# Kernel optimization log

Hardware: AMD Instinct MI355X
Metric: run time of the kernel (lower is better)

The kernel has to match this reference:

```python
import jax, jax.numpy as jnp
import numpy as np

# Module config
SIZE = (2, 2)
B, H, W, C = 16, 64, 64, 256


def setup_inputs() -> dict:
    key = jax.random.key(0)
    updates = jax.random.normal(key, (B, H, W, C), dtype=jnp.float32)
    OH, OW = H * SIZE[0], W * SIZE[1]
    # argmax-style mask: flat index into [OH, OW, C] (per-batch), pointing at the
    # top-left element of each pooling window (structure of max_pool_with_argmax)
    h = jnp.arange(H, dtype=jnp.int64)[:, None, None] * SIZE[0]   # [H,1,1]
    w = jnp.arange(W, dtype=jnp.int64)[None, :, None] * SIZE[1]   # [1,W,1]
    c = jnp.arange(C, dtype=jnp.int64)[None, None, :]             # [1,1,C]
    mask = (h * OW + w) * C + c                                   # [H,W,C]
    mask = jnp.broadcast_to(mask, (B, H, W, C))
    return {"updates": updates, "mask": mask}


def reference(updates, mask):
    # Faithful MaxUnpooling2D: scatter pooled values into upsampled output at
    # the positions given by the (per-batch flat) argmax mask; rest are zeros.
    Bv, Hv, Wv, Cv = updates.shape
    OH, OW = Hv * SIZE[0], Wv * SIZE[1]
    flat = OH * OW * Cv
    out = jnp.zeros((Bv, flat), dtype=updates.dtype)
    # tf.scatter_nd sums duplicates into a zero tensor; indices here are unique
    out = out.at[jnp.arange(Bv)[:, None], mask.reshape(Bv, -1)].add(
        updates.reshape(Bv, -1)
    )
    return out.reshape(Bv, OH, OW, Cv)
```

## Files before the change

kernel.cpp:

```cpp
#include <hip/hip_runtime.h>


constexpr int B = 16;
constexpr int H = 64, W = 64, C = 256;
constexpr int OH = 2 * H, OW = 2 * W;
constexpr long long OUT_PER_BATCH = (long long)OH * OW * C;
constexpr int N_THREADS = B * H * W * (C / 4);

typedef float f32x4 __attribute__((ext_vector_type(4)));
typedef int   i32x4 __attribute__((ext_vector_type(4)));

__global__ __launch_bounds__(256) void unpool_gather_kernel(
    const f32x4* __restrict__ upd4,
    const i32x4* __restrict__ mask4,
    float* __restrict__ out) {
    int i = blockIdx.x * blockDim.x + threadIdx.x;
    if (i >= N_THREADS) return;

    int c0 = (i & 63) << 2;
    int w  = (i >> 6) & 63;
    int h  = (i >> 12) & 63;
    int b  = i >> 18;

    i32x4 m = mask4[i];
    f32x4 u = upd4[i];

    float* obase = out + (long long)b * OUT_PER_BATCH;
    int oh = h << 1, ow = w << 1;

#pragma unroll
    for (int dy = 0; dy < 2; ++dy) {
#pragma unroll
        for (int dx = 0; dx < 2; ++dx) {
            int flat = ((oh + dy) * OW + (ow + dx)) * C + c0;
            f32x4 r;
            r.x = (m.x == flat)     ? u.x : 0.0f;
            r.y = (m.y == flat + 1) ? u.y : 0.0f;
            r.z = (m.z == flat + 2) ? u.z : 0.0f;
            r.w = (m.w == flat + 3) ? u.w : 0.0f;
            *(f32x4*)(obase + flat) = r;
        }
    }
}

extern "C" void kernel_launch(void* const* d_in, const int* in_sizes, int n_in,
                              void* d_out, int out_size, void* d_ws, size_t ws_size,
                              hipStream_t stream) {
    const f32x4* upd4  = (const f32x4*)d_in[0];
    const i32x4* mask4 = (const i32x4*)d_in[1];
    float*       out   = (float*)d_out;

    const int block = 256;
    const int grid  = N_THREADS / block;
    unpool_gather_kernel<<<grid, block, 0, stream>>>(upd4, mask4, out);
}
```

Baseline: 358.0 us.

## Switch to output-major grid-stride unpooling with contiguous vector stores

Each thread now owns one output quad and walks the output in a grid-stride loop over a fixed 2048-block grid, gathering the matching update and mask quad. Before, each thread read one input quad and wrote four scattered output quads. Now every store is perfectly contiguous across a wavefront, at the cost of reading each input quad four times (mostly from cache). The fixed grid also reduces block launch overhead.

Measured after the change: 371.2 us. 3.7% more time.

```diff
diff --git a/kernel.cpp b/kernel.cpp
--- a/kernel.cpp
+++ b/kernel.cpp
@@ -4,42 +4,38 @@
 constexpr int B = 16;
 constexpr int H = 64, W = 64, C = 256;
 constexpr int OH = 2 * H, OW = 2 * W;
-constexpr long long OUT_PER_BATCH = (long long)OH * OW * C;
-constexpr int N_THREADS = B * H * W * (C / 4);
+constexpr int N_OUT_QUADS = B * OH * OW * (C / 4);
+constexpr int GRID  = 2048;
+constexpr int BLOCK = 256;
 
 typedef float f32x4 __attribute__((ext_vector_type(4)));
 typedef int   i32x4 __attribute__((ext_vector_type(4)));
 
-__global__ __launch_bounds__(256) void unpool_gather_kernel(
+__global__ __launch_bounds__(BLOCK) void unpool_outmajor_kernel(
     const f32x4* __restrict__ upd4,
     const i32x4* __restrict__ mask4,
-    float* __restrict__ out) {
-    int i = blockIdx.x * blockDim.x + threadIdx.x;
-    if (i >= N_THREADS) return;
+    f32x4* __restrict__ out4) {
+    const int stride = GRID * BLOCK;
+    int q = blockIdx.x * BLOCK + threadIdx.x;
 
-    int c0 = (i & 63) << 2;
-    int w  = (i >> 6) & 63;
-    int h  = (i >> 12) & 63;
-    int b  = i >> 18;
+#pragma unroll 1
+    for (int it = 0; it < N_OUT_QUADS / stride; ++it, q += stride) {
+        int cq = q & 63;
+        int ow = (q >> 6) & 127;
+        int oh = (q >> 13) & 127;
+        int b  = q >> 20;
 
-    i32x4 m = mask4[i];
-    f32x4 u = upd4[i];
+        int iq = (b << 18) + ((oh >> 1) << 12) + ((ow >> 1) << 6) + cq;
+        i32x4 m = mask4[iq];
+        f32x4 u = upd4[iq];
 
-    float* obase = out + (long long)b * OUT_PER_BATCH;
-    int oh = h << 1, ow = w << 1;
-
-#pragma unroll
-    for (int dy = 0; dy < 2; ++dy) {
-#pragma unroll
-        for (int dx = 0; dx < 2; ++dx) {
-            int flat = ((oh + dy) * OW + (ow + dx)) * C + c0;
-            f32x4 r;
-            r.x = (m.x == flat)     ? u.x : 0.0f;
-            r.y = (m.y == flat + 1) ? u.y : 0.0f;
-            r.z = (m.z == flat + 2) ? u.z : 0.0f;
-            r.w = (m.w == flat + 3) ? u.w : 0.0f;
-            *(f32x4*)(obase + flat) = r;
-        }
+        int flat = (oh << 15) + (ow << 8) + (cq << 2);
+        f32x4 r;
+        r.x = (m.x == flat)     ? u.x : 0.0f;
+        r.y = (m.y == flat + 1) ? u.y : 0.0f;
+        r.z = (m.z == flat + 2) ? u.z : 0.0f;
+        r.w = (m.w == flat + 3) ? u.w : 0.0f;
+        out4[q] = r;
     }
 }
 
@@ -48,9 +44,7 @@
                               hipStream_t stream) {
     const f32x4* upd4  = (const f32x4*)d_in[0];
     const i32x4* mask4 = (const i32x4*)d_in[1];
-    float*       out   = (float*)d_out;
+    f32x4*       out4  = (f32x4*)d_out;
 
-    const int block = 256;
-    const int grid  = N_THREADS / block;
-    unpool_gather_kernel<<<grid, block, 0, stream>>>(upd4, mask4, out);
+    unpool_outmajor_kernel<<<GRID, BLOCK, 0, stream>>>(upd4, mask4, out4);
 }
```

## Replace masked gather writes with memset plus direct scatter by mask index

Applied to the files above, without the earlier changes.

Zero-fills the output with an async memset, then each thread scatters its four update values to the positions named by the mask. This drops the per-window compare logic and makes the kernel honour arbitrary mask indices. The cost is an extra pass of output traffic for the scattered writes on top of the full zero-fill, and the stores become scalar rather than 16-byte vector stores.

Result: no change. 356.9 us (-0.3%).

```diff
diff --git a/kernel.cpp b/kernel.cpp
--- a/kernel.cpp
+++ b/kernel.cpp
@@ -5,42 +5,27 @@
 constexpr int H = 64, W = 64, C = 256;
 constexpr int OH = 2 * H, OW = 2 * W;
 constexpr long long OUT_PER_BATCH = (long long)OH * OW * C;
-constexpr int N_THREADS = B * H * W * (C / 4);
+constexpr size_t OUT_BYTES = (size_t)B * OUT_PER_BATCH * sizeof(float);
+constexpr int N_QUADS = B * H * W * (C / 4);
 
 typedef float f32x4 __attribute__((ext_vector_type(4)));
 typedef int   i32x4 __attribute__((ext_vector_type(4)));
 
-__global__ __launch_bounds__(256) void unpool_gather_kernel(
+__global__ __launch_bounds__(256) void unpool_scatter4_kernel(
     const f32x4* __restrict__ upd4,
     const i32x4* __restrict__ mask4,
     float* __restrict__ out) {
     int i = blockIdx.x * blockDim.x + threadIdx.x;
-    if (i >= N_THREADS) return;
-
-    int c0 = (i & 63) << 2;
-    int w  = (i >> 6) & 63;
-    int h  = (i >> 12) & 63;
-    int b  = i >> 18;
+    int b = i >> 18;
 
     i32x4 m = mask4[i];
     f32x4 u = upd4[i];
 
     float* obase = out + (long long)b * OUT_PER_BATCH;
-    int oh = h << 1, ow = w << 1;
-
-#pragma unroll
-    for (int dy = 0; dy < 2; ++dy) {
-#pragma unroll
-        for (int dx = 0; dx < 2; ++dx) {
-            int flat = ((oh + dy) * OW + (ow + dx)) * C + c0;
-            f32x4 r;
-            r.x = (m.x == flat)     ? u.x : 0.0f;
-            r.y = (m.y == flat + 1) ? u.y : 0.0f;
-            r.z = (m.z == flat + 2) ? u.z : 0.0f;
-            r.w = (m.w == flat + 3) ? u.w : 0.0f;
-            *(f32x4*)(obase + flat) = r;
-        }
-    }
+    obase[m.x] = u.x;
+    obase[m.y] = u.y;
+    obase[m.z] = u.z;
+    obase[m.w] = u.w;
 }
 
 extern "C" void kernel_launch(void* const* d_in, const int* in_sizes, int n_in,
@@ -50,7 +35,9 @@
     const i32x4* mask4 = (const i32x4*)d_in[1];
     float*       out   = (float*)d_out;
 
+    hipMemsetAsync(out, 0, OUT_BYTES, stream);
+
     const int block = 256;
-    const int grid  = N_THREADS / block;
-    unpool_gather_kernel<<<grid, block, 0, stream>>>(upd4, mask4, out);
+    const int grid  = N_QUADS / block;
+    unpool_scatter4_kernel<<<grid, block, 0, stream>>>(upd4, mask4, out);
 }
```
